# Optimization experiments

Measured on AMD Instinct MI355X. Metric: run time of the kernel, lower is better.

The kernel has to match this reference:

```python
import jax, jax.numpy as jnp
import numpy as np

D_MODEL = 512
NUM_HEADS = 8
D_K = D_MODEL // NUM_HEADS
EPS = 1e-8


def setup_inputs() -> dict:
    key = jax.random.key(0)
    ks = jax.random.split(key, 11)
    B, N = 2, 2048
    s = 1.0 / np.sqrt(D_MODEL)
    return {
        "query": jax.random.normal(ks[0], (B, N, D_MODEL), jnp.float32),
        "key": jax.random.normal(ks[1], (B, N, D_MODEL), jnp.float32),
        "value": jax.random.normal(ks[2], (B, N, D_MODEL), jnp.float32),
        "Wq": jax.random.uniform(ks[3], (D_MODEL, D_MODEL), jnp.float32, -s, s),
        "bq": jax.random.uniform(ks[4], (D_MODEL,), jnp.float32, -s, s),
        "Wk": jax.random.uniform(ks[5], (D_MODEL, D_MODEL), jnp.float32, -s, s),
        "bk": jax.random.uniform(ks[6], (D_MODEL,), jnp.float32, -s, s),
        "Wv": jax.random.uniform(ks[7], (D_MODEL, D_MODEL), jnp.float32, -s, s),
        "bv": jax.random.uniform(ks[8], (D_MODEL,), jnp.float32, -s, s),
        "Wo": jax.random.uniform(ks[9], (D_MODEL, D_MODEL), jnp.float32, -s, s),
        "bo": jax.random.uniform(ks[10], (D_MODEL,), jnp.float32, -s, s),
    }


def _heads(x, W, b, B):
    # torch Linear: x @ W.T + b ; then [B,N,H,dk] -> [B,H,N,dk]
    y = x @ W.T + b
    return y.reshape(B, -1, NUM_HEADS, D_K).transpose(0, 2, 1, 3)


def reference(query, key, value, Wq, bq, Wk, bk, Wv, bv, Wo, bo):
    B = query.shape[0]
    Q = _heads(query, Wq, bq, B)
    K = _heads(key, Wk, bk, B)
    V = _heads(value, Wv, bv, B)
    # elu(x) + 1 feature map
    Q = jax.nn.elu(Q) + 1.0
    K = jax.nn.elu(K) + 1.0
    # normalize Q over feature dim, K over sequence dim
    Qn = Q / (Q.sum(axis=-1, keepdims=True) + EPS)
    Kn = K / (K.sum(axis=-2, keepdims=True) + EPS)
    # explicit NxN context matrix (as in the original code)
    attention_weights = jnp.einsum("bhnd,bhmd->bhnm", Qn, Kn)  # [B,H,N,N]
    out = jnp.einsum("bhnm,bhmd->bhnd", attention_weights, V)   # [B,H,N,dk]
    out = out.transpose(0, 2, 1, 3).reshape(B, -1, D_MODEL)
    out = out @ Wo.T + bo
    return (out, attention_weights)
```

## Files before the change

### kernel.cpp

```cpp
#include <hip/hip_runtime.h>
#include <math.h>

#define NSEQ  2048
#define DM    512
#define NH    8
#define DK    64
#define MROWS 4096
#define BH    16
#define BHSTR (NSEQ*DK)
#define SLAB  (BH*BHSTR)
#define EPSF  1e-8f
#define OUT0  (MROWS*DM)

typedef __attribute__((ext_vector_type(8))) short short8;
typedef __attribute__((ext_vector_type(4))) float f32x4;
union S8 { short8 v; short s[8]; };
union F4 { f32x4 v; float f[4]; };

__device__ short g_qh[MROWS*DM], g_ql[MROWS*DM];
__device__ short g_kh[MROWS*DM], g_kl[MROWS*DM];
__device__ short g_vh[MROWS*DM];
__device__ short g_wqh[DM*DM], g_wql[DM*DM];
__device__ short g_wkh[DM*DM], g_wkl[DM*DM];
__device__ short g_wvh[DM*DM], g_woh[DM*DM];
__device__ unsigned short g_Qbf[SLAB];
__device__ unsigned short g_Kbf[SLAB];
__device__ float          g_Vf[SLAB];
__device__ short          g_OHbf[MROWS*DM];
__device__ float          g_qinv[BH*NSEQ];
__device__ float          g_ksum[BH*DK];
__device__ float          g_KV[BH*DK*DK];

__device__ __forceinline__ unsigned short f2bf(float x) {
    union { float f; unsigned u; } v; v.f = x;
    unsigned r = v.u + 0x7fffu + ((v.u >> 16) & 1u);
    return (unsigned short)(r >> 16);
}
__device__ __forceinline__ float bf2f(unsigned short h) {
    union { unsigned u; float f; } v; v.u = ((unsigned)h) << 16; return v.f;
}
__device__ __forceinline__ f32x4 mfma_bf16(short8 a, short8 b, f32x4 c) {
    return __builtin_amdgcn_mfma_f32_16x16x32_bf16(a, b, c, 0, 0, 0);
}
__device__ __forceinline__ float elu1(float x) {
    return (x > 0.f) ? (x + 1.f) : __expf(x);
}
__device__ __forceinline__ void gl_lds16(const void* gsrc, void* ldst) {
    __builtin_amdgcn_global_load_lds(
        (__attribute__((address_space(1))) void*)(unsigned long long)(gsrc),
        (__attribute__((address_space(3))) void*)(unsigned)(unsigned long long)(ldst),
        16, 0, 0);
}

__global__ __launch_bounds__(256) void prep_kernel(const float* __restrict__ q, const float* __restrict__ k,
                                                   const float* __restrict__ v, const float* __restrict__ wq,
                                                   const float* __restrict__ wk, const float* __restrict__ wv,
                                                   const float* __restrict__ wo) {
    int b = blockIdx.x, t = threadIdx.x;
    if (b < 33) {
        int z = b * 2048 + t * 8;
#pragma unroll
        for (int i = 0; i < 8; i++) {
            int zz = z + i;
            if (zz < 65536) g_KV[zz] = 0.f;
            else if (zz < 66560) g_ksum[zz - 65536] = 0.f;
        }
    }
    const float* src; short* hi; short* lo; int off; int split;
    if (b < 1024)      { src = q;  hi = g_qh;  lo = g_ql;  off = b * 2048;          split = 1; }
    else if (b < 2048) { src = k;  hi = g_kh;  lo = g_kl;  off = (b-1024) * 2048;   split = 1; }
    else if (b < 3072) { src = v;  hi = g_vh;  lo = g_vh;  off = (b-2048) * 2048;   split = 0; }
    else if (b < 3200) { src = wq; hi = g_wqh; lo = g_wql; off = (b-3072) * 2048;   split = 1; }
    else if (b < 3328) { src = wk; hi = g_wkh; lo = g_wkl; off = (b-3200) * 2048;   split = 1; }
    else if (b < 3456) { src = wv; hi = g_wvh; lo = g_wvh; off = (b-3328) * 2048;   split = 0; }
    else               { src = wo; hi = g_woh; lo = g_woh; off = (b-3456) * 2048;   split = 0; }
    int idx = off + t * 8;
    F4 a0, a1; a0.v = *(const f32x4*)(src + idx); a1.v = *(const f32x4*)(src + idx + 4);
    S8 h, l;
#pragma unroll
    for (int i = 0; i < 4; i++) {
        unsigned short hb = f2bf(a0.f[i]); h.s[i] = (short)hb;
        l.s[i] = (short)f2bf(a0.f[i] - bf2f(hb));
    }
#pragma unroll
    for (int i = 0; i < 4; i++) {
        unsigned short hb = f2bf(a1.f[i]); h.s[4+i] = (short)hb;
        l.s[4+i] = (short)f2bf(a1.f[i] - bf2f(hb));
    }
    *(short8*)(hi + idx) = h.v;
    if (split) *(short8*)(lo + idx) = l.v;
}

template<int SPLIT>
__global__ __launch_bounds__(256) void gemm_bf16(const float* __restrict__ bias,
                                                 float* __restrict__ dout, int mode) {
    __shared__ short sAh[128*64];
    __shared__ short sBh[64*64];
    __shared__ short sAl[SPLIT ? 128*64 : 8];
    __shared__ short sBl[SPLIT ? 64*64 : 8];

    const short *Ahi, *Alo = nullptr, *Bhi, *Blo = nullptr;
    if (mode == 0)      { Ahi = g_qh;   Alo = g_ql;  Bhi = g_wqh; Blo = g_wql; }
    else if (mode == 1) { Ahi = g_kh;   Alo = g_kl;  Bhi = g_wkh; Blo = g_wkl; }
    else if (mode == 2) { Ahi = g_vh;   Bhi = g_wvh; }
    else                { Ahi = g_OHbf; Bhi = g_woh; }

    int t = threadIdx.x, lane = t & 63, w = t >> 6;
    int l15 = lane & 15, quad = lane >> 4;
    int m0 = blockIdx.x * 128, n0 = blockIdx.y * 64;
    int r_in = lane >> 3, gq = lane & 7;
    int scol = (gq ^ r_in) << 3;

    f32x4 acc[2][4];
    f32x4 z4 = {0.f, 0.f, 0.f, 0.f};
#pragma unroll
    for (int i = 0; i < 2; i++)
#pragma unroll
        for (int j = 0; j < 4; j++) acc[i][j] = z4;

    for (int k0 = 0; k0 < 512; k0 += 64) {
#pragma unroll
        for (int ii = 0; ii < 4; ii++) {
            int i = w * 4 + ii;
            size_t so = (size_t)(m0 + i*8 + r_in) * 512 + k0 + scol;
            gl_lds16(Ahi + so, &sAh[i * 512]);
            if (SPLIT) gl_lds16(Alo + so, &sAl[i * 512]);
        }
#pragma unroll
        for (int ii = 0; ii < 2; ii++) {
            int i = w * 2 + ii;
            size_t so = (size_t)(n0 + i*8 + r_in) * 512 + k0 + scol;
            gl_lds16(Bhi + so, &sBh[i * 512]);
            if (SPLIT) gl_lds16(Blo + so, &sBl[i * 512]);
        }
        __syncthreads();

#pragma unroll
        for (int ks = 0; ks < 2; ks++) {
            int kg = ks * 4 + quad;
            int sw = (kg ^ (l15 & 7)) << 3;
            short8 ah[2], al[2], bh[4], bl[4];
#pragma unroll
            for (int i = 0; i < 2; i++) {
                int ad = (w*32 + i*16 + l15) * 64 + sw;
                ah[i] = *(const short8*)&sAh[ad];
                if (SPLIT) al[i] = *(const short8*)&sAl[ad];
            }
#pragma unroll
            for (int j = 0; j < 4; j++) {
                int ad = (j*16 + l15) * 64 + sw;
                bh[j] = *(const short8*)&sBh[ad];
                if (SPLIT) bl[j] = *(const short8*)&sBl[ad];
            }
#pragma unroll
            for (int i = 0; i < 2; i++)
#pragma unroll
                for (int j = 0; j < 4; j++) {
                    acc[i][j] = mfma_bf16(ah[i], bh[j], acc[i][j]);
                    if (SPLIT) {
                        acc[i][j] = mfma_bf16(ah[i], bl[j], acc[i][j]);
                        acc[i][j] = mfma_bf16(al[i], bh[j], acc[i][j]);
                    }
                }
        }
        __syncthreads();
    }

    int head = blockIdx.y;
    int bh16 = ((m0 >> 11) << 3) + head;
    if (mode == 3) {
#pragma unroll
        for (int j = 0; j < 4; j++) {
            int col = n0 + j*16 + l15;
            float bsv = bias[col];
#pragma unroll
            for (int i = 0; i < 2; i++) {
                F4 v; v.v = acc[i][j];
#pragma unroll
                for (int r = 0; r < 4; r++) {
                    int row = m0 + w*32 + i*16 + quad*4 + r;
                    dout[(size_t)row * 512 + col] = v.f[r] + bsv;
                }
            }
        }
    } else if (mode == 2) {
#pragma unroll
        for (int j = 0; j < 4; j++) {
            int col = n0 + j*16 + l15;
            float bsv = bias[col];
            int dd = col & 63;
#pragma unroll
            for (int i = 0; i < 2; i++) {
                F4 v; v.v = acc[i][j];
#pragma unroll
                for (int r = 0; r < 4; r++) {
                    int nn = (m0 + w*32 + i*16 + quad*4 + r) & 2047;
                    g_Vf[(size_t)bh16 * BHSTR + nn*64 + dd] = v.f[r] + bsv;
                }
            }
        }
    } else {
        float e[2][4][4];
#pragma unroll
        for (int j = 0; j < 4; j++) {
            float bsv = bias[n0 + j*16 + l15];
#pragma unroll
            for (int i = 0; i < 2; i++) {
                F4 v; v.v = acc[i][j];
#pragma unroll
                for (int r = 0; r < 4; r++) e[i][j][r] = elu1(v.f[r] + bsv);
            }
        }
        if (mode == 0) {
            float rks[4];
#pragma unroll
            for (int j = 0; j < 4; j++)
                rks[j] = 1.f / (g_ksum[bh16*64 + j*16 + l15] + EPSF);
#pragma unroll
            for (int i = 0; i < 2; i++) {
#pragma unroll
                for (int r = 0; r < 4; r++) {
                    float s = e[i][0][r] + e[i][1][r] + e[i][2][r] + e[i][3][r];
                    s += __shfl_xor(s, 1); s += __shfl_xor(s, 2);
                    s += __shfl_xor(s, 4); s += __shfl_xor(s, 8);
                    if (l15 == 0) {
                        int nn = (m0 + w*32 + i*16 + quad*4 + r) & 2047;
                        g_qinv[bh16*NSEQ + nn] = 1.f / (s + EPSF);
                    }
                }
#pragma unroll
                for (int j = 0; j < 4; j++) {
                    int dd = j*16 + l15;
#pragma unroll
                    for (int r = 0; r < 4; r++) {
                        int nn = (m0 + w*32 + i*16 + quad*4 + r) & 2047;
                        g_Qbf[(size_t)bh16 * BHSTR + nn*64 + dd] = f2bf(e[i][j][r] * rks[j]);
                    }
                }
            }
        } else {
#pragma unroll
            for (int j = 0; j < 4; j++) {
                int dd = j*16 + l15;
                float s = 0.f;
#pragma unroll
                for (int i = 0; i < 2; i++)
#pragma unroll
                    for (int r = 0; r < 4; r++) {
                        int nn = (m0 + w*32 + i*16 + quad*4 + r) & 2047;
                        g_Kbf[(size_t)bh16 * BHSTR + nn*64 + dd] = f2bf(e[i][j][r]);
                        s += e[i][j][r];
                    }
                s += __shfl_xor(s, 16); s += __shfl_xor(s, 32);
                if (lane < 16) atomicAdd(&g_ksum[bh16*64 + dd], s);
            }
        }
    }
}

__global__ __launch_bounds__(256) void attn_kernel(float* __restrict__ dout) {
    __shared__ __align__(16) char smem[64*132*4];
    short* Qs = (short*)smem;
    short* Ks = (short*)(smem + 16384);
    float* Ts = (float*)smem;

    int bh = blockIdx.z;
    int m0 = blockIdx.x * 128, n0 = blockIdx.y * 128;
    int t = threadIdx.x, lane = t & 63, w = t >> 6;
    int l15 = lane & 15, quad = lane >> 4;
    int r_in = lane >> 3, gq = lane & 7;
    int scol = (gq ^ r_in) << 3;

    const short* qb = (const short*)g_Qbf + (size_t)bh * BHSTR;
    const short* kb = (const short*)g_Kbf + (size_t)bh * BHSTR;
#pragma unroll
    for (int ii = 0; ii < 4; ii++) {
        int i = w * 4 + ii;
        gl_lds16(qb + (size_t)(m0 + i*8 + r_in) * 64 + scol, &Qs[i * 512]);
        gl_lds16(kb + (size_t)(n0 + i*8 + r_in) * 64 + scol, &Ks[i * 512]);
    }
    __syncthreads();

    int wm = (w >> 1) * 64, wn = (w & 1) * 64;
    f32x4 acc[4][4];
    f32x4 z4 = {0.f, 0.f, 0.f, 0.f};
#pragma unroll
    for (int i = 0; i < 4; i++)
#pragma unroll
        for (int j = 0; j < 4; j++) acc[i][j] = z4;

#pragma unroll
    for (int ks = 0; ks < 2; ks++) {
        int kg = ks * 4 + quad;
        int sw = (kg ^ (l15 & 7)) << 3;
        short8 qa[4], kbf[4];
#pragma unroll
        for (int i = 0; i < 4; i++) qa[i]  = *(const short8*)&Qs[(wm + i*16 + l15) * 64 + sw];
#pragma unroll
        for (int j = 0; j < 4; j++) kbf[j] = *(const short8*)&Ks[(wn + j*16 + l15) * 64 + sw];
#pragma unroll
        for (int i = 0; i < 4; i++)
#pragma unroll
            for (int j = 0; j < 4; j++) acc[i][j] = mfma_bf16(qa[i], kbf[j], acc[i][j]);
    }

    float* outp = dout + OUT0 + (size_t)bh * NSEQ * NSEQ;
    int halfw = w >> 1;
    int l31 = lane & 31, lh = lane >> 5;

#pragma unroll
    for (int h = 0; h < 2; h++) {
        __syncthreads();
        if (halfw == h) {
#pragma unroll
            for (int i = 0; i < 4; i++) {
#pragma unroll
                for (int r2 = 0; r2 < 4; r2++) {
                    int row_l = i*16 + quad*4 + r2;
                    float qiv = g_qinv[bh*NSEQ + m0 + h*64 + row_l];
#pragma unroll
                    for (int j = 0; j < 4; j++) {
                        F4 v; v.v = acc[i][j];
                        Ts[row_l*132 + wn + j*16 + l15] = v.f[r2] * qiv;
                    }
                }
            }
        }
        __syncthreads();
#pragma unroll
        for (int rr = 0; rr < 8; rr++) {
            int row_l = w*16 + rr*2 + lh;
            f32x4 val = *(const f32x4*)&Ts[row_l*132 + l31*4];
            int grow = m0 + h*64 + row_l;
            __builtin_nontemporal_store(val, (f32x4*)(outp + (size_t)grow * NSEQ + n0 + l31*4));
        }
    }
}

__global__ __launch_bounds__(256) void kv_kernel() {
    __shared__ float Ks2[64*64], Vs[64*64];
    int bh = blockIdx.x >> 4, part = blockIdx.x & 15;
    int t = threadIdx.x, d = t & 63, e0 = (t >> 6) * 16;
    float accv[16];
#pragma unroll
    for (int i = 0; i < 16; i++) accv[i] = 0.f;
    int sr = t >> 2, sc = (t & 3) * 16;
    for (int c = 0; c < 2; c++) {
        int nbase = part * 128 + c * 64;
        const unsigned short* kgp = g_Kbf + (size_t)bh * BHSTR + (size_t)(nbase + sr) * 64 + sc;
        const float* vgp = g_Vf + (size_t)bh * BHSTR + (size_t)(nbase + sr) * 64 + sc;
        S8 k0, k1;
        k0.v = *(const short8*)(kgp);
        k1.v = *(const short8*)(kgp + 8);
#pragma unroll
        for (int i = 0; i < 8; i++) Ks2[sr*64 + sc + i]     = bf2f((unsigned short)k0.s[i]);
#pragma unroll
        for (int i = 0; i < 8; i++) Ks2[sr*64 + sc + 8 + i] = bf2f((unsigned short)k1.s[i]);
#pragma unroll
        for (int i = 0; i < 4; i++) *(f32x4*)&Vs[sr*64 + sc + 4*i] = *(const f32x4*)(vgp + 4*i);
        __syncthreads();
#pragma unroll 4
        for (int m = 0; m < 64; m++) {
            float v = Vs[m*64 + d];
            const f32x4* kr = (const f32x4*)&Ks2[m*64 + e0];
            F4 q0, q1, q2, q3;
            q0.v = kr[0]; q1.v = kr[1]; q2.v = kr[2]; q3.v = kr[3];
#pragma unroll
            for (int i = 0; i < 4; i++) accv[i]      += q0.f[i] * v;
#pragma unroll
            for (int i = 0; i < 4; i++) accv[4 + i]  += q1.f[i] * v;
#pragma unroll
            for (int i = 0; i < 4; i++) accv[8 + i]  += q2.f[i] * v;
#pragma unroll
            for (int i = 0; i < 4; i++) accv[12 + i] += q3.f[i] * v;
        }
        __syncthreads();
    }
#pragma unroll
    for (int i = 0; i < 16; i++)
        atomicAdd(&g_KV[bh*4096 + (e0 + i)*64 + d], accv[i]);
}

__global__ __launch_bounds__(256) void oh_kernel() {
    __shared__ float Qs2[128*64];
    __shared__ float KVs[64*64];
    int bh = blockIdx.y, r0 = blockIdx.x * 128;
    int t = threadIdx.x, d = t & 63, w = t >> 6;
    {
        int r = t >> 2, c = (t & 3) * 16;
        const float* s = g_KV + bh*4096 + r*64 + c;
#pragma unroll
        for (int i = 0; i < 4; i++) *(f32x4*)&KVs[r*64 + c + 4*i] = *(const f32x4*)(s + 4*i);
    }
    {
        int r = t >> 1, c = (t & 1) * 32;
        const unsigned short* s = g_Qbf + (size_t)bh * BHSTR + (size_t)(r0 + r) * 64 + c;
#pragma unroll
        for (int i = 0; i < 4; i++) {
            S8 x; x.v = *(const short8*)(s + 8*i);
#pragma unroll
            for (int j = 0; j < 8; j++) Qs2[r*64 + c + 8*i + j] = bf2f((unsigned short)x.s[j]);
        }
    }
    __syncthreads();
    float kvc[64];
#pragma unroll
    for (int e = 0; e < 64; e++) kvc[e] = KVs[e*64 + d];
    int b = bh >> 3, h = bh & 7;
    for (int rr = 0; rr < 32; rr++) {
        int row = w * 32 + rr;
        const f32x4* qr = (const f32x4*)&Qs2[row*64];
        float a = 0.f;
#pragma unroll
        for (int e4 = 0; e4 < 16; e4++) {
            F4 q; q.v = qr[e4];
            a += q.f[0]*kvc[4*e4] + q.f[1]*kvc[4*e4+1] + q.f[2]*kvc[4*e4+2] + q.f[3]*kvc[4*e4+3];
        }
        int grow = r0 + row;
        float val = a * g_qinv[bh*NSEQ + grow];
        g_OHbf[((size_t)b*NSEQ + grow)*512 + h*64 + d] = (short)f2bf(val);
    }
}

extern "C" void kernel_launch(void* const* d_in, const int* in_sizes, int n_in,
                              void* d_out, int out_size, void* d_ws, size_t ws_size,
                              hipStream_t stream) {
    const float* q  = (const float*)d_in[0];
    const float* k  = (const float*)d_in[1];
    const float* v  = (const float*)d_in[2];
    const float* Wq = (const float*)d_in[3];
    const float* bq = (const float*)d_in[4];
    const float* Wk = (const float*)d_in[5];
    const float* bk = (const float*)d_in[6];
    const float* Wv = (const float*)d_in[7];
    const float* bv = (const float*)d_in[8];
    const float* Wo = (const float*)d_in[9];
    const float* bo = (const float*)d_in[10];
    float* out = (float*)d_out;

    prep_kernel<<<3584, 256, 0, stream>>>(q, k, v, Wq, Wk, Wv, Wo);

    dim3 gproj(32, 8);
    gemm_bf16<1><<<gproj, 256, 0, stream>>>(bk, nullptr, 1);
    gemm_bf16<1><<<gproj, 256, 0, stream>>>(bq, nullptr, 0);
    gemm_bf16<0><<<gproj, 256, 0, stream>>>(bv, nullptr, 2);

    attn_kernel<<<dim3(16, 16, BH), 256, 0, stream>>>(out);

    kv_kernel<<<256, 256, 0, stream>>>();
    oh_kernel<<<dim3(16, BH), 256, 0, stream>>>();

    gemm_bf16<0><<<gproj, 256, 0, stream>>>(bo, out, 3);
}
```

Before: 394.6 us.

## Merge K and V projection launches and remap attention block order per XCD

The GEMM template is made runtime-moded so the K and V projections run in one launch with blockIdx.z choosing the mode, which cuts a launch and fills more CUs per wave. The attention kernel remaps the flat block id so that consecutive blocks scheduled round-robin across the 8 XCDs share the same (bh, tile) neighbourhood, aiming for better L2 locality. The cost is that the runtime split flag and full-size low-part LDS buffers may raise register and LDS use for the non-split modes and lower occupancy.

```diff
diff --git a/kernel.cpp b/kernel.cpp
--- a/kernel.cpp
+++ b/kernel.cpp
@@ -91,13 +91,18 @@
     if (split) *(short8*)(lo + idx) = l.v;
 }
 
-template<int SPLIT>
-__global__ __launch_bounds__(256) void gemm_bf16(const float* __restrict__ bias,
-                                                 float* __restrict__ dout, int mode) {
+__global__ __launch_bounds__(256) void gemm_bf16(const float* __restrict__ biasA,
+                                                 const float* __restrict__ biasB,
+                                                 float* __restrict__ dout,
+                                                 int modeA, int modeB) {
     __shared__ short sAh[128*64];
     __shared__ short sBh[64*64];
-    __shared__ short sAl[SPLIT ? 128*64 : 8];
-    __shared__ short sBl[SPLIT ? 64*64 : 8];
+    __shared__ short sAl[128*64];
+    __shared__ short sBl[64*64];
+
+    int mode = (blockIdx.z == 0) ? modeA : modeB;
+    const float* bias = (blockIdx.z == 0) ? biasA : biasB;
+    const int split = (mode == 0 || mode == 1);
 
     const short *Ahi, *Alo = nullptr, *Bhi, *Blo = nullptr;
     if (mode == 0)      { Ahi = g_qh;   Alo = g_ql;  Bhi = g_wqh; Blo = g_wql; }
@@ -124,14 +129,14 @@
             int i = w * 4 + ii;
             size_t so = (size_t)(m0 + i*8 + r_in) * 512 + k0 + scol;
             gl_lds16(Ahi + so, &sAh[i * 512]);
-            if (SPLIT) gl_lds16(Alo + so, &sAl[i * 512]);
+            if (split) gl_lds16(Alo + so, &sAl[i * 512]);
         }
 #pragma unroll
         for (int ii = 0; ii < 2; ii++) {
             int i = w * 2 + ii;
             size_t so = (size_t)(n0 + i*8 + r_in) * 512 + k0 + scol;
             gl_lds16(Bhi + so, &sBh[i * 512]);
-            if (SPLIT) gl_lds16(Blo + so, &sBl[i * 512]);
+            if (split) gl_lds16(Blo + so, &sBl[i * 512]);
         }
         __syncthreads();
 
@@ -144,20 +149,20 @@
             for (int i = 0; i < 2; i++) {
                 int ad = (w*32 + i*16 + l15) * 64 + sw;
                 ah[i] = *(const short8*)&sAh[ad];
-                if (SPLIT) al[i] = *(const short8*)&sAl[ad];
+                if (split) al[i] = *(const short8*)&sAl[ad];
             }
 #pragma unroll
             for (int j = 0; j < 4; j++) {
                 int ad = (j*16 + l15) * 64 + sw;
                 bh[j] = *(const short8*)&sBh[ad];
-                if (SPLIT) bl[j] = *(const short8*)&sBl[ad];
+                if (split) bl[j] = *(const short8*)&sBl[ad];
             }
 #pragma unroll
             for (int i = 0; i < 2; i++)
 #pragma unroll
                 for (int j = 0; j < 4; j++) {
                     acc[i][j] = mfma_bf16(ah[i], bh[j], acc[i][j]);
-                    if (SPLIT) {
+                    if (split) {
                         acc[i][j] = mfma_bf16(ah[i], bl[j], acc[i][j]);
                         acc[i][j] = mfma_bf16(al[i], bh[j], acc[i][j]);
                     }
@@ -264,8 +269,12 @@
     short* Ks = (short*)(smem + 16384);
     float* Ts = (float*)smem;
 
-    int bh = blockIdx.z;
-    int m0 = blockIdx.x * 128, n0 = blockIdx.y * 128;
+    int fid = blockIdx.x + (blockIdx.y << 4) + (blockIdx.z << 8);
+    int sid = (fid & 7) * 512 + (fid >> 3);
+    int bh = sid >> 8;
+    int m0 = (sid & 15) << 7;
+    int n0 = ((sid >> 4) & 15) << 7;
+
     int t = threadIdx.x, lane = t & 63, w = t >> 6;
     int l15 = lane & 15, quad = lane >> 4;
     int r_in = lane >> 3, gq = lane & 7;
@@ -440,15 +449,13 @@
 
     prep_kernel<<<3584, 256, 0, stream>>>(q, k, v, Wq, Wk, Wv, Wo);
 
-    dim3 gproj(32, 8);
-    gemm_bf16<1><<<gproj, 256, 0, stream>>>(bk, nullptr, 1);
-    gemm_bf16<1><<<gproj, 256, 0, stream>>>(bq, nullptr, 0);
-    gemm_bf16<0><<<gproj, 256, 0, stream>>>(bv, nullptr, 2);
+    gemm_bf16<<<dim3(32, 8, 2), 256, 0, stream>>>(bk, bv, nullptr, 1, 2);
+    gemm_bf16<<<dim3(32, 8, 1), 256, 0, stream>>>(bq, bq, nullptr, 0, 0);
 
     attn_kernel<<<dim3(16, 16, BH), 256, 0, stream>>>(out);
 
     kv_kernel<<<256, 256, 0, stream>>>();
     oh_kernel<<<dim3(16, BH), 256, 0, stream>>>();
 
-    gemm_bf16<0><<<gproj, 256, 0, stream>>>(bo, out, 3);
-}
+    gemm_bf16<<<dim3(32, 8, 1), 256, 0, stream>>>(bo, bo, out, 3, 3);
+}
```

New measurement: 392.4 us. Within noise of the previous version (-0.6%).
